# Kernel tuning notes

Measured on AMD Instinct MI355X. Metric: run time of the kernel, lower is better.

The kernel has to match this reference:

```python
import jax, jax.numpy as jnp
import numpy as np

NUM_HEADS = 8
EPS = 1e-12  # torch F.normalize eps


def setup_inputs() -> dict:
    key = jax.random.key(0)
    k1, k2, k3 = jax.random.split(key, 3)
    b, c, h, w = 4, 384, 128, 128
    x = jax.random.normal(k1, (b, c, h, w), dtype=jnp.float32)
    qkv_w = jax.random.normal(k2, (3 * c, c), dtype=jnp.float32) * (1.0 / np.sqrt(c))
    proj_w = jax.random.normal(k3, (c, c), dtype=jnp.float32) * (1.0 / np.sqrt(c))
    temperature = jnp.ones((NUM_HEADS, 1, 1), dtype=jnp.float32)
    return {"x": x, "qkv_w": qkv_w, "proj_w": proj_w, "temperature": temperature}


def _l2_normalize(t):
    # matches torch F.normalize(dim=-1): t / max(||t||_2, eps)
    n = jnp.sqrt(jnp.sum(t * t, axis=-1, keepdims=True))
    return t / jnp.maximum(n, EPS)


def reference(x, qkv_w, proj_w, temperature):
    b, c, h, w = x.shape
    heads = NUM_HEADS
    ch = c // heads  # per-head channel dim
    n = h * w
    # 1x1 conv == channel matmul
    qkv = jnp.einsum('bchw,oc->bohw', x, qkv_w)          # [b, 3c, h, w]
    qkv = qkv.reshape(b, 3, heads, ch, n)                # split qkv / heads / flatten spatial
    q, k, v = qkv[:, 0], qkv[:, 1], qkv[:, 2]            # [b, heads, ch, n]
    q = _l2_normalize(q)
    k = _l2_normalize(k)
    attn = jnp.einsum('bhcn,bhdn->bhcd', q, k) * temperature  # [b, heads, ch, ch]
    attn = jax.nn.softmax(attn, axis=-1)
    out = jnp.einsum('bhcd,bhdn->bhcn', attn, v)         # [b, heads, ch, n]
    out = out.reshape(b, c, h, w)
    out = jnp.einsum('bchw,oc->bohw', out, proj_w)       # 1x1 projection
    return out
```

## Files before the change

### kernel.cpp

```cpp
#include <hip/hip_runtime.h>
#include <stdint.h>

#define HW 16384
#define CH 384
#define NS 32

typedef float  f32x4  __attribute__((ext_vector_type(4)));
typedef short  short8 __attribute__((ext_vector_type(8)));
typedef __bf16 bf16x8 __attribute__((ext_vector_type(8)));
typedef unsigned short u16;
typedef u16 u16x4 __attribute__((ext_vector_type(4)));

__device__ __forceinline__ u16 f2bf(float f) {
  union { float f; uint32_t u; } v; v.f = f;
  uint32_t r = v.u + 0x7fffu + ((v.u >> 16) & 1u);
  return (u16)(r >> 16);
}
__device__ __forceinline__ float bf2f(u16 v) {
  union { uint32_t u; float f; } x; x.u = ((uint32_t)v) << 16; return x.f;
}
__device__ __forceinline__ f32x4 zero4() { f32x4 z = {0.f, 0.f, 0.f, 0.f}; return z; }

__device__ __forceinline__ f32x4 mfma_bf16(short8 a, short8 b, f32x4 c) {
  return __builtin_amdgcn_mfma_f32_16x16x32_bf16(
      __builtin_bit_cast(bf16x8, a), __builtin_bit_cast(bf16x8, b), c, 0, 0, 0);
}

__device__ __forceinline__ void gload16(const void* g, void* lds) {
  auto gp = (const __attribute__((address_space(1))) uint32_t*)(uintptr_t)g;
  auto lp = (__attribute__((address_space(3))) uint32_t*)(uintptr_t)lds;
  __builtin_amdgcn_global_load_lds(gp, lp, 16, 0, 0);
}

__global__ void k_convert_w(const float* __restrict__ w, u16* __restrict__ o) {
  int i = blockIdx.x * 256 + threadIdx.x;
  if (i < 1152 * CH) o[i] = f2bf(w[i]);
}

__global__ __launch_bounds__(256) void k_wvt(const float* __restrict__ w,
                                             u16* __restrict__ wvt) {
  __shared__ u16 tl[64][72];
  const int ci = blockIdx.x, di = blockIdx.y, t = threadIdx.x;
#pragma unroll
  for (int jj = 0; jj < 4; ++jj) {
    const int r = (t >> 4) + jj * 16;
    f32x4 v = *(const f32x4*)(w + (size_t)(768 + di * 64 + r) * CH + ci * 64 + (t & 15) * 4);
#pragma unroll
    for (int i = 0; i < 4; ++i) tl[(t & 15) * 4 + i][r] = f2bf(v[i]);
  }
  __syncthreads();
#pragma unroll
  for (int jj = 0; jj < 2; ++jj) {
    const int c = (t >> 3) + jj * 32;
    short8 v = *(const short8*)(&tl[c][(t & 7) * 8]);
    *(short8*)(wvt + (size_t)(ci * 64 + c) * CH + di * 64 + (t & 7) * 8) = v;
  }
}

__global__ __launch_bounds__(256) void k_transpose_x(const float* __restrict__ x,
                                                     u16* __restrict__ xT,
                                                     u16* __restrict__ xb) {
  __shared__ u16 tile[64][72];
  const int b = blockIdx.z, c0 = blockIdx.y * 64, n0 = blockIdx.x * 64;
  const int t = threadIdx.x;
  const float* xp = x + (size_t)b * CH * HW;
  u16* xbp = xb + (size_t)b * CH * HW;
  const int nq = t & 15;
  const int cr = t >> 4;
#pragma unroll
  for (int jj = 0; jj < 4; ++jj) {
    const int c = cr + jj * 16;
    f32x4 v = *(const f32x4*)(xp + (size_t)(c0 + c) * HW + n0 + nq * 4);
    u16x4 pk;
#pragma unroll
    for (int i = 0; i < 4; ++i) { u16 bv = f2bf(v[i]); tile[nq * 4 + i][c] = bv; pk[i] = bv; }
    *(u16x4*)(xbp + (size_t)(c0 + c) * HW + n0 + nq * 4) = pk;
  }
  __syncthreads();
  u16* xtb = xT + (size_t)b * HW * CH;
  const int cc = t & 7;
  const int r0 = t >> 3;
#pragma unroll
  for (int jj = 0; jj < 2; ++jj) {
    const int r = r0 + jj * 32;
    short8 v = *(const short8*)(&tile[r][cc * 8]);
    *(short8*)(xtb + (size_t)(n0 + r) * CH + c0 + cc * 8) = v;
  }
}

template <int STRIDE>
__device__ __forceinline__ void stageS(u16* lds, const u16* __restrict__ g, int t) {
  const int w = t >> 6;
#pragma unroll
  for (int s = 0; s < 2; ++s) {
    const int r = s * 32 + (t >> 3);
    const int g8 = (t & 7) ^ (r & 7);
    const int gr = 2 * r + (g8 >> 2);
    gload16(g + (size_t)gr * STRIDE + (g8 & 3) * 8, lds + s * 2048 + w * 512);
  }
}

__global__ __launch_bounds__(256) void k_gramx(const u16* __restrict__ xb,
                                               float* __restrict__ part) {
  const int orig = blockIdx.x;
  const int L = (orig & 7) * (6 * NS * 4 / 8) + (orig >> 3);
  const int pair = L % 6;
  const int ns = (L / 6) % NS;
  const int b = L / (6 * NS);
  const int i = pair < 3 ? 0 : (pair < 5 ? 1 : 2);
  const int j = pair < 3 ? pair : (pair < 5 ? pair - 2 : 2);
  const int t = threadIdx.x, lane = t & 63, w = t >> 6;
  const int wo = w & 1, wn = w >> 1;
  const u16* pa = xb + ((size_t)b * CH + i * 128) * HW + ns * 512;
  const u16* pb = xb + ((size_t)b * CH + j * 128) * HW + ns * 512;

  __shared__ u16 As[3][64 * 64];
  __shared__ u16 Bs[3][64 * 64];

  f32x4 acc[4][4];
#pragma unroll
  for (int a = 0; a < 4; ++a)
#pragma unroll
    for (int c = 0; c < 4; ++c) acc[a][c] = zero4();

#pragma unroll
  for (int p = 0; p < 2; ++p) {
    stageS<HW>(As[p], pa + p * 32, t);
    stageS<HW>(Bs[p], pb + p * 32, t);
  }
  const int ks = lane >> 4;
  for (int kt = 0; kt < 16; ++kt) {
    if (kt < 15) asm volatile("s_waitcnt vmcnt(4)" ::: "memory");
    else         asm volatile("s_waitcnt vmcnt(0)" ::: "memory");
    asm volatile("s_barrier" ::: "memory");
    if (kt <= 13) {
      stageS<HW>(As[(kt + 2) % 3], pa + (kt + 2) * 32, t);
      stageS<HW>(Bs[(kt + 2) % 3], pb + (kt + 2) * 32, t);
    }
    const u16* Ac = As[kt % 3];
    const u16* Bc = Bs[kt % 3];
    short8 af[4], bf[4];
#pragma unroll
    for (int mi = 0; mi < 4; ++mi) {
      const int gr = wo * 64 + mi * 16 + (lane & 15);
      const int r = gr >> 1;
      const int p = ((gr & 1) * 4 + ks) ^ (r & 7);
      af[mi] = *(const short8*)(Ac + r * 64 + p * 8);
    }
#pragma unroll
    for (int ni = 0; ni < 4; ++ni) {
      const int gr = wn * 64 + ni * 16 + (lane & 15);
      const int r = gr >> 1;
      const int p = ((gr & 1) * 4 + ks) ^ (r & 7);
      bf[ni] = *(const short8*)(Bc + r * 64 + p * 8);
    }
#pragma unroll
    for (int ni = 0; ni < 4; ++ni)
#pragma unroll
      for (int mi = 0; mi < 4; ++mi)
        acc[ni][mi] = mfma_bf16(bf[ni], af[mi], acc[ni][mi]);
  }
  float* dst = part + ((size_t)(b * 6 + pair) * NS + ns) * 16384;
#pragma unroll
  for (int ni = 0; ni < 4; ++ni)
#pragma unroll
    for (int mi = 0; mi < 4; ++mi) {
      const int ai = wo * 64 + mi * 16 + (lane & 15);
      const int bj = wn * 64 + ni * 16 + ((lane >> 4) << 2);
      *(f32x4*)(dst + (size_t)ai * 128 + bj) = acc[ni][mi];
    }
}

__global__ __launch_bounds__(256) void k_greduce(const float* __restrict__ part,
                                                 u16* __restrict__ Goff,
                                                 float* __restrict__ Gd) {
  const int cq = blockIdx.x, pair = blockIdx.y, b = blockIdx.z;
  const int i = pair < 3 ? 0 : (pair < 5 ? 1 : 2);
  const int j = pair < 3 ? pair : (pair < 5 ? pair - 2 : 2);
  const int t = threadIdx.x;
  const int c0 = cq * 32;
  __shared__ u16 tl[32][136];
  const float* src = part + (size_t)(b * 6 + pair) * NS * 16384;
#pragma unroll
  for (int p = 0; p < 4; ++p) {
    const int q = t + p * 256;
    const int ai = q >> 3;
    const int bj = c0 + (q & 7) * 4;
    f32x4 s = zero4();
    for (int ns = 0; ns < NS; ++ns) s += *(const f32x4*)(src + (size_t)ns * 16384 + ai * 128 + bj);
    if (i == j) {
#pragma unroll
      for (int jj = 0; jj < 4; ++jj)
        if (ai == bj + jj) { Gd[b * CH + i * 128 + ai] = s[jj]; s[jj] = 0.f; }
    }
    u16x4 pk;
#pragma unroll
    for (int jj = 0; jj < 4; ++jj) { pk[jj] = f2bf(s[jj]); tl[bj - c0 + jj][ai] = pk[jj]; }
    *(u16x4*)(Goff + ((size_t)b * CH + i * 128 + ai) * CH + j * 128 + bj) = pk;
  }
  if (i != j) {
    __syncthreads();
#pragma unroll
    for (int jj = 0; jj < 2; ++jj) {
      const int r = t >> 3;
      const int ch = ((t & 7) + jj * 8) * 8;
      short8 v = *(const short8*)(&tl[r][ch]);
      *(short8*)(Goff + ((size_t)b * CH + j * 128 + c0 + r) * CH + i * 128 + ch) = v;
    }
  }
}

template <int TM>
__global__ __launch_bounds__(256) void k_mini(const u16* __restrict__ A,
                                              const u16* __restrict__ B,
                                              float* __restrict__ Tout,
                                              u16* __restrict__ Bout,
                                              const float* __restrict__ Gd,
                                              const u16* __restrict__ Wd) {
  const int nt = blockIdx.x, mt = blockIdx.y, b = blockIdx.z;
  __shared__ u16 Ws[4][64 * 64];
  __shared__ u16 Xs[4][64 * 64];
  const int t = threadIdx.x, lane = t & 63, w = t >> 6;
  const int wo = w & 1, wn = w >> 1;
  const u16* Ab = A + (TM ? 0 : (size_t)b * CH * CH) + (size_t)mt * 128 * CH;
  const u16* Bb = B + (TM ? (size_t)b * CH * CH : 0) + (size_t)nt * 128 * CH;

  f32x4 acc[4][4];
#pragma unroll
  for (int a = 0; a < 4; ++a)
#pragma unroll
    for (int c = 0; c < 4; ++c) acc[a][c] = zero4();

#pragma unroll
  for (int p = 0; p < 3; ++p) {
    stageS<CH>(Ws[p], Ab + p * 32, t);
    stageS<CH>(Xs[p], Bb + p * 32, t);
  }
  const int ks = lane >> 4;
  for (int kt = 0; kt < 12; ++kt) {
    if (kt <= 9)       asm volatile("s_waitcnt vmcnt(8)" ::: "memory");
    else if (kt == 10) asm volatile("s_waitcnt vmcnt(4)" ::: "memory");
    else               asm volatile("s_waitcnt vmcnt(0)" ::: "memory");
    asm volatile("s_barrier" ::: "memory");
    if (kt < 9) {
      stageS<CH>(Ws[(kt + 3) & 3], Ab + (kt + 3) * 32, t);
      stageS<CH>(Xs[(kt + 3) & 3], Bb + (kt + 3) * 32, t);
    }
    const u16* Wc = Ws[kt & 3];
    const u16* Xc = Xs[kt & 3];
    short8 af[4], bfr[4];
#pragma unroll
    for (int mi = 0; mi < 4; ++mi) {
      const int gr = wo * 64 + mi * 16 + (lane & 15);
      const int r = gr >> 1;
      const int p = ((gr & 1) * 4 + ks) ^ (r & 7);
      af[mi] = *(const short8*)(Wc + r * 64 + p * 8);
    }
#pragma unroll
    for (int ni = 0; ni < 4; ++ni) {
      const int gr = wn * 64 + ni * 16 + (lane & 15);
      const int r = gr >> 1;
      const int p = ((gr & 1) * 4 + ks) ^ (r & 7);
      bfr[ni] = *(const short8*)(Xc + r * 64 + p * 8);
    }
#pragma unroll
    for (int ni = 0; ni < 4; ++ni)
#pragma unroll
      for (int mi = 0; mi < 4; ++mi)
        acc[ni][mi] = mfma_bf16(bfr[ni], af[mi], acc[ni][mi]);
  }

#pragma unroll
  for (int ni = 0; ni < 4; ++ni)
#pragma unroll
    for (int mi = 0; mi < 4; ++mi) {
      const int tr = mt * 128 + wo * 64 + mi * 16 + (lane & 15);
      const int d0 = nt * 128 + wn * 64 + ni * 16 + ((lane >> 4) << 2);
      if (TM) {
        f32x4 g = *(const f32x4*)(Gd + b * CH + d0);
        u16x4 w4 = *(const u16x4*)(Wd + (size_t)tr * CH + d0);
        f32x4 v;
#pragma unroll
        for (int jj = 0; jj < 4; ++jj) v[jj] = acc[ni][mi][jj] + bf2f(w4[jj]) * g[jj];
        *(f32x4*)(Tout + ((size_t)b * 768 + tr) * CH + d0) = v;
      } else {
        u16x4 pk;
#pragma unroll
        for (int jj = 0; jj < 4; ++jj) pk[jj] = f2bf(acc[ni][mi][jj]);
        *(u16x4*)(Bout + ((size_t)b * CH + tr) * CH + d0) = pk;
      }
    }
}

__global__ __launch_bounds__(384) void k_attn(const float* __restrict__ T,
                                              const u16* __restrict__ wbf,
                                              const float* __restrict__ projw,
                                              const float* __restrict__ temp,
                                              u16* __restrict__ Mbf) {
  const int h = blockIdx.x, b = blockIdx.y, t = threadIdx.x;
  __shared__ float Sl[48][48];
  __shared__ float attn[48][48];
  __shared__ float nrm[96];
  const float* T1 = T + ((size_t)b * 768 + h * 48) * CH;
  const float* T2 = T1 + (size_t)384 * CH;
  const u16* wk = wbf + (size_t)(384 + h * 48) * CH;

  if (t < 64) {
    const int lane = t;
    f32x4 sa[3][3];
#pragma unroll
    for (int a = 0; a < 3; ++a)
#pragma unroll
      for (int c = 0; c < 3; ++c) sa[a][c] = zero4();
    for (int kk = 0; kk < 12; ++kk) {
      const int kc = kk * 32 + ((lane >> 4) << 3);
      short8 afr[3], bfr[3];
#pragma unroll
      for (int mi = 0; mi < 3; ++mi) {
        const float* s = T1 + (size_t)(mi * 16 + (lane & 15)) * CH + kc;
        f32x4 v0 = *(const f32x4*)(s);
        f32x4 v1 = *(const f32x4*)(s + 4);
        short8 a;
#pragma unroll
        for (int jj = 0; jj < 4; ++jj) { a[jj] = (short)f2bf(v0[jj]); a[4 + jj] = (short)f2bf(v1[jj]); }
        afr[mi] = a;
      }
#pragma unroll
      for (int ni = 0; ni < 3; ++ni)
        bfr[ni] = *(const short8*)(wk + (size_t)(ni * 16 + (lane & 15)) * CH + kc);
#pragma unroll
      for (int ni = 0; ni < 3; ++ni)
#pragma unroll
        for (int mi = 0; mi < 3; ++mi)
          sa[ni][mi] = mfma_bf16(bfr[ni], afr[mi], sa[ni][mi]);
    }
#pragma unroll
    for (int ni = 0; ni < 3; ++ni)
#pragma unroll
      for (int mi = 0; mi < 3; ++mi)
#pragma unroll
        for (int jj = 0; jj < 4; ++jj)
          Sl[mi * 16 + (lane & 15)][ni * 16 + ((lane >> 4) << 2) + jj] = sa[ni][mi][jj];
  } else if (t < 160) {
    const int r = t - 64;
    const float* Tr = (r < 48) ? T1 + (size_t)r * CH : T2 + (size_t)(r - 48) * CH;
    const u16* wr = (r < 48) ? wbf + (size_t)(h * 48 + r) * CH
                             : wbf + (size_t)(384 + h * 48 + (r - 48)) * CH;
    float a = 0.f;
    for (int c4 = 0; c4 < 96; ++c4) {
      f32x4 tv = *(const f32x4*)(Tr + c4 * 4);
      u16x4 wv = *(const u16x4*)(wr + c4 * 4);
#pragma unroll
      for (int jj = 0; jj < 4; ++jj) a = fmaf(tv[jj], bf2f(wv[jj]), a);
    }
    nrm[r] = a;
  }
  __syncthreads();
  if (t < 48) {
    const float th = temp[h];
    const float inq = 1.f / fmaxf(sqrtf(nrm[t]), 1e-12f);
    float l[48];
    float mx = -3.4e38f;
#pragma unroll
    for (int u = 0; u < 48; ++u) {
      float ik = 1.f / fmaxf(sqrtf(nrm[48 + u]), 1e-12f);
      float lg = Sl[t][u] * inq * ik * th;
      l[u] = lg;
      mx = fmaxf(mx, lg);
    }
    float sum = 0.f;
#pragma unroll
    for (int u = 0; u < 48; ++u) { float e = __expf(l[u] - mx); l[u] = e; sum += e; }
    float inv = 1.f / sum;
#pragma unroll
    for (int u = 0; u < 48; ++u) attn[t][u] = l[u] * inv;
  }
  __syncthreads();
  float pw[48];
#pragma unroll
  for (int c = 0; c < 48; ++c) pw[c] = projw[(size_t)t * CH + h * 48 + c];
  u16* Mb = Mbf + ((size_t)b * CH + t) * CH + h * 48;
#pragma unroll 4
  for (int d = 0; d < 48; ++d) {
    float a = 0.f;
#pragma unroll
    for (int c = 0; c < 48; ++c) a = fmaf(pw[c], attn[c][d], a);
    Mb[d] = f2bf(a);
  }
}

__global__ __launch_bounds__(256) void k_final(const u16* __restrict__ P,
                                               const u16* __restrict__ Bx,
                                               float* __restrict__ outp) {
  constexpr int NWG = 3 * 128 * 4;
  constexpr int CHUNK = NWG / 8;
  const int orig = blockIdx.x;
  const int L = (orig & 7) * CHUNK + (orig >> 3);
  const int ot = L % 3;
  const int ntg = L / 3;
  const int b = ntg >> 7;
  const int nt = ntg & 127;

  __shared__ u16 Ws[4][64 * 64];
  __shared__ u16 Xs[4][64 * 64];
  const int t = threadIdx.x, lane = t & 63, w = t >> 6;
  const int wo = w & 1, wn = w >> 1;
  const u16* Ab = P + (size_t)b * CH * CH + (size_t)ot * 128 * CH;
  const u16* Bb = Bx + (size_t)b * HW * CH + (size_t)nt * 128 * CH;

  f32x4 acc[4][4];
#pragma unroll
  for (int a = 0; a < 4; ++a)
#pragma unroll
    for (int c = 0; c < 4; ++c) acc[a][c] = zero4();

#pragma unroll
  for (int p = 0; p < 3; ++p) {
    stageS<CH>(Ws[p], Ab + p * 32, t);
    stageS<CH>(Xs[p], Bb + p * 32, t);
  }
  const int ks = lane >> 4;
  for (int kt = 0; kt < 12; ++kt) {
    if (kt <= 9)       asm volatile("s_waitcnt vmcnt(8)" ::: "memory");
    else if (kt == 10) asm volatile("s_waitcnt vmcnt(4)" ::: "memory");
    else               asm volatile("s_waitcnt vmcnt(0)" ::: "memory");
    asm volatile("s_barrier" ::: "memory");
    if (kt < 9) {
      stageS<CH>(Ws[(kt + 3) & 3], Ab + (kt + 3) * 32, t);
      stageS<CH>(Xs[(kt + 3) & 3], Bb + (kt + 3) * 32, t);
    }
    const u16* Wc = Ws[kt & 3];
    const u16* Xc = Xs[kt & 3];
    short8 af[4], bfr[4];
#pragma unroll
    for (int mi = 0; mi < 4; ++mi) {
      const int gr = wo * 64 + mi * 16 + (lane & 15);
      const int r = gr >> 1;
      const int p = ((gr & 1) * 4 + ks) ^ (r & 7);
      af[mi] = *(const short8*)(Wc + r * 64 + p * 8);
    }
#pragma unroll
    for (int ni = 0; ni < 4; ++ni) {
      const int gr = wn * 64 + ni * 16 + (lane & 15);
      const int r = gr >> 1;
      const int p = ((gr & 1) * 4 + ks) ^ (r & 7);
      bfr[ni] = *(const short8*)(Xc + r * 64 + p * 8);
    }
#pragma unroll
    for (int ni = 0; ni < 4; ++ni)
#pragma unroll
      for (int mi = 0; mi < 4; ++mi)
        acc[ni][mi] = mfma_bf16(bfr[ni], af[mi], acc[ni][mi]);
  }
  float* ob = outp + (size_t)b * CH * HW;
#pragma unroll
  for (int ni = 0; ni < 4; ++ni)
#pragma unroll
    for (int mi = 0; mi < 4; ++mi) {
      int o = ot * 128 + wo * 64 + mi * 16 + (lane & 15);
      int n = nt * 128 + wn * 64 + ni * 16 + ((lane >> 4) << 2);
      *(f32x4*)(ob + (size_t)o * HW + n) = acc[ni][mi];
    }
}

extern "C" void kernel_launch(void* const* d_in, const int* in_sizes, int n_in,
                              void* d_out, int out_size, void* d_ws, size_t ws_size,
                              hipStream_t stream) {
  const float* x     = (const float*)d_in[0];
  const float* qkvw  = (const float*)d_in[1];
  const float* projw = (const float*)d_in[2];
  const float* temp  = (const float*)d_in[3];
  float* out = (float*)d_out;
  char* ws = (char*)d_ws;

  u16*   xT   = (u16*)(ws);
  u16*   wbf  = (u16*)(ws + 50331648);
  u16*   wvt  = (u16*)(ws + 51216384);
  u16*   Goff = (u16*)(ws + 51511296);
  float* Gd   = (float*)(ws + 52690944);
  float* Tf   = (float*)(ws + 52697088);
  u16*   Mbf  = (u16*)(ws + 57415680);
  u16*   Pbf  = (u16*)(ws + 58595328);
  u16*   xb   = (u16*)d_out;
  float* part = (float*)((char*)d_out + 50331648);

  k_convert_w<<<dim3((1152 * CH + 255) / 256), 256, 0, stream>>>(qkvw, wbf);
  k_wvt<<<dim3(6, 6), 256, 0, stream>>>(qkvw, wvt);
  k_transpose_x<<<dim3(HW / 64, CH / 64, 4), 256, 0, stream>>>(x, xT, xb);
  k_gramx<<<dim3(6 * NS * 4), 256, 0, stream>>>(xb, part);
  k_greduce<<<dim3(4, 6, 4), 256, 0, stream>>>(part, Goff, Gd);
  k_mini<1><<<dim3(3, 6, 4), 256, 0, stream>>>(wbf, Goff, Tf, nullptr, Gd, wbf);
  k_attn<<<dim3(8, 4), 384, 0, stream>>>(Tf, wbf, projw, temp, Mbf);
  k_mini<0><<<dim3(3, 3, 4), 256, 0, stream>>>(Mbf, wvt, nullptr, Pbf, nullptr, nullptr);
  k_final<<<dim3(3 * 128 * 4), 256, 0, stream>>>(Pbf, xT, out);
}
```

Baseline: 156.5 us.

## Keep full X tile resident in LDS and loop over output tiles in k_final

k_final now has one workgroup per (spatial tile, batch). It loads the whole 128x384 bf16 X slice into LDS once with a swizzled layout, then iterates over the three 128-row output tiles, streaming only P through a triple buffer. This removes the threefold reloading of X across output tiles. The cost is about 120KB of LDS per block, which lowers occupancy, and a grid of only 512 blocks. Padding of the transpose tiles in k_wvt and k_transpose_x also shrinks from 72 to 66.

```diff
diff --git a/kernel.cpp b/kernel.cpp
--- a/kernel.cpp
+++ b/kernel.cpp
@@ -39,7 +39,7 @@
 
 __global__ __launch_bounds__(256) void k_wvt(const float* __restrict__ w,
                                              u16* __restrict__ wvt) {
-  __shared__ u16 tl[64][72];
+  __shared__ u16 tl[64][66];
   const int ci = blockIdx.x, di = blockIdx.y, t = threadIdx.x;
 #pragma unroll
   for (int jj = 0; jj < 4; ++jj) {
@@ -60,7 +60,7 @@
 __global__ __launch_bounds__(256) void k_transpose_x(const float* __restrict__ x,
                                                      u16* __restrict__ xT,
                                                      u16* __restrict__ xb) {
-  __shared__ u16 tile[64][72];
+  __shared__ u16 tile[64][66];
   const int b = blockIdx.z, c0 = blockIdx.y * 64, n0 = blockIdx.x * 64;
   const int t = threadIdx.x;
   const float* xp = x + (size_t)b * CH * HW;
@@ -392,75 +392,68 @@
 __global__ __launch_bounds__(256) void k_final(const u16* __restrict__ P,
                                                const u16* __restrict__ Bx,
                                                float* __restrict__ outp) {
-  constexpr int NWG = 3 * 128 * 4;
-  constexpr int CHUNK = NWG / 8;
-  const int orig = blockIdx.x;
-  const int L = (orig & 7) * CHUNK + (orig >> 3);
-  const int ot = L % 3;
-  const int ntg = L / 3;
-  const int b = ntg >> 7;
-  const int nt = ntg & 127;
-
-  __shared__ u16 Ws[4][64 * 64];
-  __shared__ u16 Xs[4][64 * 64];
+  const int nt = blockIdx.x, b = blockIdx.y;
+  __shared__ u16 Bs[128 * 384];
+  __shared__ u16 As[3][64 * 64];
   const int t = threadIdx.x, lane = t & 63, w = t >> 6;
   const int wo = w & 1, wn = w >> 1;
-  const u16* Ab = P + (size_t)b * CH * CH + (size_t)ot * 128 * CH;
   const u16* Bb = Bx + (size_t)b * HW * CH + (size_t)nt * 128 * CH;
+  const u16* Pb = P + (size_t)b * CH * CH;
+
+  for (int i = 0; i < 24; ++i) {
+    const int id = i * 256 + t;
+    const int r = id / 48, p = id % 48;
+    const int gp = (p & ~7) | ((p & 7) ^ (r & 7));
+    gload16(Bb + (size_t)r * CH + gp * 8, Bs + i * 2048 + w * 512);
+  }
+  const int ks = lane >> 4;
 
   f32x4 acc[4][4];
-#pragma unroll
-  for (int a = 0; a < 4; ++a)
-#pragma unroll
-    for (int c = 0; c < 4; ++c) acc[a][c] = zero4();
-
-#pragma unroll
-  for (int p = 0; p < 3; ++p) {
-    stageS<CH>(Ws[p], Ab + p * 32, t);
-    stageS<CH>(Xs[p], Bb + p * 32, t);
-  }
-  const int ks = lane >> 4;
-  for (int kt = 0; kt < 12; ++kt) {
-    if (kt <= 9)       asm volatile("s_waitcnt vmcnt(8)" ::: "memory");
-    else if (kt == 10) asm volatile("s_waitcnt vmcnt(4)" ::: "memory");
-    else               asm volatile("s_waitcnt vmcnt(0)" ::: "memory");
-    asm volatile("s_barrier" ::: "memory");
-    if (kt < 9) {
-      stageS<CH>(Ws[(kt + 3) & 3], Ab + (kt + 3) * 32, t);
-      stageS<CH>(Xs[(kt + 3) & 3], Bb + (kt + 3) * 32, t);
-    }
-    const u16* Wc = Ws[kt & 3];
-    const u16* Xc = Xs[kt & 3];
-    short8 af[4], bfr[4];
-#pragma unroll
-    for (int mi = 0; mi < 4; ++mi) {
-      const int gr = wo * 64 + mi * 16 + (lane & 15);
-      const int r = gr >> 1;
-      const int p = ((gr & 1) * 4 + ks) ^ (r & 7);
-      af[mi] = *(const short8*)(Wc + r * 64 + p * 8);
-    }
-#pragma unroll
-    for (int ni = 0; ni < 4; ++ni) {
-      const int gr = wn * 64 + ni * 16 + (lane & 15);
-      const int r = gr >> 1;
-      const int p = ((gr & 1) * 4 + ks) ^ (r & 7);
-      bfr[ni] = *(const short8*)(Xc + r * 64 + p * 8);
-    }
+  for (int ot = 0; ot < 3; ++ot) {
+    const u16* Ab = Pb + (size_t)ot * 128 * CH;
+#pragma unroll
+    for (int a = 0; a < 4; ++a)
+#pragma unroll
+      for (int c = 0; c < 4; ++c) acc[a][c] = zero4();
+    stageS<CH>(As[0], Ab, t);
+    stageS<CH>(As[1], Ab + 32, t);
+    for (int kt = 0; kt < 12; ++kt) {
+      if (kt < 11) asm volatile("s_waitcnt vmcnt(2)" ::: "memory");
+      else         asm volatile("s_waitcnt vmcnt(0)" ::: "memory");
+      asm volatile("s_barrier" ::: "memory");
+      if (kt < 10) stageS<CH>(As[(kt + 2) % 3], Ab + (kt + 2) * 32, t);
+      const u16* Ac = As[kt % 3];
+      short8 af[4], bfr[4];
+#pragma unroll
+      for (int mi = 0; mi < 4; ++mi) {
+        const int gr = wo * 64 + mi * 16 + (lane & 15);
+        const int r = gr >> 1;
+        const int p = ((gr & 1) * 4 + ks) ^ (r & 7);
+        af[mi] = *(const short8*)(Ac + r * 64 + p * 8);
+      }
+#pragma unroll
+      for (int ni = 0; ni < 4; ++ni) {
+        const int gr = wn * 64 + ni * 16 + (lane & 15);
+        const int ck = kt * 4 + ks;
+        const int cp = (ck & ~7) | ((ck & 7) ^ (gr & 7));
+        bfr[ni] = *(const short8*)(Bs + (size_t)gr * CH + cp * 8);
+      }
+#pragma unroll
+      for (int ni = 0; ni < 4; ++ni)
+#pragma unroll
+        for (int mi = 0; mi < 4; ++mi)
+          acc[ni][mi] = mfma_bf16(bfr[ni], af[mi], acc[ni][mi]);
+    }
+    float* ob = outp + (size_t)b * CH * HW;
 #pragma unroll
     for (int ni = 0; ni < 4; ++ni)
 #pragma unroll
-      for (int mi = 0; mi < 4; ++mi)
-        acc[ni][mi] = mfma_bf16(bfr[ni], af[mi], acc[ni][mi]);
-  }
-  float* ob = outp + (size_t)b * CH * HW;
-#pragma unroll
-  for (int ni = 0; ni < 4; ++ni)
-#pragma unroll
-    for (int mi = 0; mi < 4; ++mi) {
-      int o = ot * 128 + wo * 64 + mi * 16 + (lane & 15);
-      int n = nt * 128 + wn * 64 + ni * 16 + ((lane >> 4) << 2);
-      *(f32x4*)(ob + (size_t)o * HW + n) = acc[ni][mi];
-    }
+      for (int mi = 0; mi < 4; ++mi) {
+        int o = ot * 128 + wo * 64 + mi * 16 + (lane & 15);
+        int n = nt * 128 + wn * 64 + ni * 16 + ((lane >> 4) << 2);
+        *(f32x4*)(ob + (size_t)o * HW + n) = acc[ni][mi];
+      }
+  }
 }
 
 extern "C" void kernel_launch(void* const* d_in, const int* in_sizes, int n_in,
@@ -492,5 +485,5 @@
   k_mini<1><<<dim3(3, 6, 4), 256, 0, stream>>>(wbf, Goff, Tf, nullptr, Gd, wbf);
   k_attn<<<dim3(8, 4), 384, 0, stream>>>(Tf, wbf, projw, temp, Mbf);
   k_mini<0><<<dim3(3, 3, 4), 256, 0, stream>>>(Mbf, wvt, nullptr, Pbf, nullptr, nullptr);
-  k_final<<<dim3(3 * 128 * 4), 256, 0, stream>>>(Pbf, xT, out);
-}
+  k_final<<<dim3(128, 4), 256, 0, stream>>>(Pbf, xT, out);
+}
```

Result: slower. 160.8 us (+2.8%).
